# Kernel tuning notes

Hardware: AMD Instinct MI355X
Metric: run time of the kernel (lower is better)

The kernel has to match this reference:

```python
import jax, jax.numpy as jnp
import numpy as np

FACTOR = 5

def setup_inputs() -> dict:
    key = jax.random.key(0)
    k1, k2, k3, k4 = jax.random.split(key, 4)
    B, L, H, D = 4, 2048, 8, 64
    sample_k = min(FACTOR * int(np.ceil(np.log(L))), L)  # 40
    return {
        "queries": jax.random.normal(k1, (B, L, H, D), dtype=jnp.float32),
        "keys": jax.random.normal(k2, (B, L, H, D), dtype=jnp.float32),
        "values": jax.random.normal(k3, (B, L, H, D), dtype=jnp.float32),
        "index_sample": jax.random.randint(k4, (L, sample_k), 0, L, dtype=jnp.int32),
    }

def reference(queries, keys, values, index_sample):
    # [B, L, H, D] -> [B, H, L, D]
    Q = jnp.transpose(queries, (0, 2, 1, 3))
    K = jnp.transpose(keys, (0, 2, 1, 3))
    V = jnp.transpose(values, (0, 2, 1, 3))
    B, H, L_Q, D = Q.shape
    L_K = K.shape[2]
    u = min(FACTOR * int(np.ceil(np.log(L_Q))), L_Q)  # n_top

    # --- _prob_QK: sampled QK scores ---
    # K_sample: [B, H, L_Q, sample_k, D]
    K_sample = K[:, :, index_sample, :]
    # Q_K_sample[b,h,l,s] = Q[b,h,l,:] . K_sample[b,h,l,s,:]
    Q_K_sample = jnp.einsum('bhld,bhlsd->bhls', Q, K_sample)
    # sparsity measure M: max - mean over L_K
    M = Q_K_sample.max(axis=-1) - Q_K_sample.sum(axis=-1) / L_K  # [B,H,L_Q]
    _, M_top = jax.lax.top_k(M, u)  # [B,H,u]

    # reduced Q -> full scores against all keys
    Q_reduce = jnp.take_along_axis(Q, M_top[..., None], axis=2)  # [B,H,u,D]
    scores = jnp.einsum('bhud,bhkd->bhuk', Q_reduce, K)  # [B,H,u,L_K]
    scale = 1.0 / jnp.sqrt(jnp.asarray(D, dtype=scores.dtype))
    scores = scores * scale

    # --- initial context: mean of V over keys (mask_flag=False) ---
    V_mean = V.mean(axis=-2)  # [B,H,D]
    context = jnp.broadcast_to(V_mean[:, :, None, :], (B, H, L_Q, D))

    # --- update context at top-u query positions ---
    attn = jax.nn.softmax(scores, axis=-1)  # [B,H,u,L_K]
    ctx_top = jnp.einsum('bhuk,bhkd->bhud', attn, V)  # [B,H,u,D]
    b_idx = jnp.arange(B)[:, None, None]
    h_idx = jnp.arange(H)[None, :, None]
    context = context.at[b_idx, h_idx, M_top].set(ctx_top)
    return context  # [B, H, L_Q, D]
```

## Files before the change

kernel.cpp:

```cpp
#include <hip/hip_runtime.h>
#include <math.h>

#define LL 2048
#define HH 8
#define DD 64
#define SK 40
#define UU 40
#define SCALE 0.125f

__device__ __forceinline__ float dot4(float4 a, float4 b) {
  return a.x * b.x + a.y * b.y + a.z * b.z + a.w * b.w;
}


__global__ __launch_bounds__(512, 4) void k_A(
    const float* __restrict__ Q, const float* __restrict__ K,
    const float* __restrict__ V, const int* __restrict__ idxs,
    float* __restrict__ Mout, float* __restrict__ part)
{
  int bx = blockIdx.x;
  int t = threadIdx.x;

  if (bx < 2048) {
    __shared__ int sidx[4 * SK];
    __shared__ float wred[2][4][2][8];

    int xcd = bx & 7, slot = bx >> 3;
    int b = xcd >> 1;
    int l0 = ((xcd & 1) << 10) | (slot << 2);
    int w = t >> 6, lane = t & 63;
    int lpos = w >> 1, half = w & 1;
    int l = l0 + lpos;
    int h = (lane >> 2) & 7, dg = lane & 3, sp = lane >> 5;

    if (t < 4 * SK) sidx[t] = idxs[l0 * SK + t];

    const float4* Q4 = (const float4*)Q;
    int qb = (((b << 11) + l) << 7) + (h << 4) + dg;
    float4 q0 = Q4[qb], q1 = Q4[qb + 4], q2 = Q4[qb + 8], q3 = Q4[qb + 12];

    const float4* K4 = (const float4*)K;
    int kbb = (b << 18) + (h << 4) + dg;

    __syncthreads();

    const int* hidx = &sidx[lpos * SK + half * 20];
    float mx = -INFINITY, sum = 0.f;
#pragma unroll
    for (int pp = 0; pp < 10; pp += 2) {
      int i0 = hidx[pp * 2 + sp];
      int i1 = hidx[pp * 2 + 2 + sp];
      int o0 = kbb + (i0 << 7);
      int o1 = kbb + (i1 << 7);
      float4 a0 = K4[o0], a1 = K4[o0 + 4], a2 = K4[o0 + 8], a3 = K4[o0 + 12];
      float4 c0 = K4[o1], c1 = K4[o1 + 4], c2 = K4[o1 + 8], c3 = K4[o1 + 12];
      float p = dot4(q0, a0) + dot4(q1, a1) + dot4(q2, a2) + dot4(q3, a3);
      float r = dot4(q0, c0) + dot4(q1, c1) + dot4(q2, c2) + dot4(q3, c3);
      p += __shfl_xor(p, 1); p += __shfl_xor(p, 2);
      r += __shfl_xor(r, 1); r += __shfl_xor(r, 2);
      mx = fmaxf(mx, fmaxf(p, r));
      sum += p + r;
    }
    mx = fmaxf(mx, __shfl_xor(mx, 32));
    sum += __shfl_xor(sum, 32);
    if ((lane & 35) == 0) {
      wred[0][lpos][half][h] = mx;
      wred[1][lpos][half][h] = sum;
    }
    __syncthreads();
    if (t < 32) {
      int lp = t >> 3, hh = t & 7;
      float M0 = fmaxf(wred[0][lp][0][hh], wred[0][lp][1][hh]);
      float S0 = wred[1][lp][0][hh] + wred[1][lp][1][hh];
      Mout[((b * HH + hh) << 11) + (l0 + lp)] = M0 - S0 * (1.0f / (float)LL);
    }
  } else {
    __shared__ float sm[8][64];
    int blk = bx - 2048;
    int bh = blk >> 3, c = blk & 7;
    int b = bh >> 3, h = bh & 7;
    int w = t >> 6, d = t & 63;
    int l0 = (c << 8) + (w << 5);
    int base = (b << 20) + (l0 << 9) + (h << 6) + d;
    float a0 = 0, a1 = 0, a2 = 0, a3 = 0;
#pragma unroll
    for (int j = 0; j < 32; j += 4) {
      a0 += V[base + ((j + 0) << 9)];
      a1 += V[base + ((j + 1) << 9)];
      a2 += V[base + ((j + 2) << 9)];
      a3 += V[base + ((j + 3) << 9)];
    }
    sm[w][d] = a0 + a1 + a2 + a3;
    __syncthreads();
    if (t < 64) {
      float s = 0;
#pragma unroll
      for (int i = 0; i < 8; ++i) s += sm[i][t];
      part[(blk << 6) + t] = s;
    }
  }
}

__global__ __launch_bounds__(256) void k_B(
    const float* __restrict__ Mv, int* __restrict__ Mtop,
    const float4* __restrict__ part4, float4* __restrict__ out4)
{
  int bx = blockIdx.x;
  int t = threadIdx.x;

  if (bx < 32) {
    __shared__ float sv[LL];
    __shared__ float wm[4];
    __shared__ int wi[4];
    int bh = bx;
    int w = t >> 6, ln = t & 63;
    for (int i = t; i < LL; i += 256) sv[i] = Mv[bh * LL + i];
    __syncthreads();
    for (int r = 0; r < UU; ++r) {
      float bv = -INFINITY; int bi = 0;
#pragma unroll
      for (int j = 0; j < 8; ++j) {
        int i = t + (j << 8);
        float v = sv[i];
        if (v > bv) { bv = v; bi = i; }
      }
#pragma unroll
      for (int off = 1; off < 64; off <<= 1) {
        float ov = __shfl_xor(bv, off);
        int oi = __shfl_xor(bi, off);
        if (ov > bv || (ov == bv && oi < bi)) { bv = ov; bi = oi; }
      }
      if (ln == 0) { wm[w] = bv; wi[w] = bi; }
      __syncthreads();
      if (t == 0) {
        float Bv = wm[0]; int Bi = wi[0];
#pragma unroll
        for (int k = 1; k < 4; ++k)
          if (wm[k] > Bv || (wm[k] == Bv && wi[k] < Bi)) { Bv = wm[k]; Bi = wi[k]; }
        Mtop[bh * UU + r] = Bi;
        sv[Bi] = -INFINITY;
      }
      __syncthreads();
    }
  } else {
    __shared__ float4 vm[16];
    int i = (bx - 32) * 256 + t;
    int bh = i >> 15;
    if (t < 16) {
      int d4 = t;
      float4 s = {0, 0, 0, 0};
#pragma unroll
      for (int c = 0; c < 8; ++c) {
        float4 p = part4[((bh << 3) + c) * 16 + d4];
        s.x += p.x; s.y += p.y; s.z += p.z; s.w += p.w;
      }
      const float inv = 1.0f / (float)LL;
      s.x *= inv; s.y *= inv; s.z *= inv; s.w *= inv;
      vm[d4] = s;
    }
    __syncthreads();
    out4[i] = vm[i & 15];
  }
}

__global__ __launch_bounds__(512) void k_attn2(
    const float* __restrict__ Q, const float* __restrict__ K,
    const float* __restrict__ V, const int* __restrict__ Mtop,
    float* __restrict__ pm, float* __restrict__ pl, float4* __restrict__ pO4)
{
  __shared__ float4 Ks4[1024];
  __shared__ float Ps[8][256];
  __shared__ float4 Os4[4][2][4][16];
  __shared__ int gqi[8];

  int bx = blockIdx.x;
  int ch = bx & 7;
  int slot = bx >> 3;
  int bh = slot / 5, rg = slot % 5;
  int b = bh >> 3, h = bh & 7;
  int t = threadIdx.x;
  int w = t >> 6, ln = t & 63;
  int l0 = ch << 8;

  if (t < 8) gqi[t] = Mtop[bh * UU + rg * 8 + t];
  __syncthreads();

  float4 qv[16];
  {
    const float4* qrow = (const float4*)Q + (((b << 11) + gqi[w]) << 7) + (h << 4);
#pragma unroll
    for (int i = 0; i < 16; ++i) qv[i] = qrow[i];
  }

  const float4* K4 = (const float4*)K;
  int kbase = (((b << 11) + l0) << 7) + (h << 4);
  int col0 = t >> 4, d40 = t & 15;
  int sw0 = col0 * 16 + (d40 ^ (col0 & 7));
  float4 g0 = K4[kbase + col0 * 128 + d40];
  float4 g1 = K4[kbase + (col0 + 32) * 128 + d40];

  float sc[4];
#pragma unroll
  for (int st = 0; st < 4; ++st) {
    __syncthreads();
    Ks4[sw0] = g0;
    Ks4[sw0 + 512] = g1;
    float4 n0, n1;
    if (st < 3) {
      int lr = (st + 1) * 64;
      n0 = K4[kbase + (lr + col0) * 128 + d40];
      n1 = K4[kbase + (lr + col0 + 32) * 128 + d40];
    }
    __syncthreads();
    float s = 0.f;
#pragma unroll
    for (int d4 = 0; d4 < 16; ++d4) {
      float4 kv = Ks4[ln * 16 + (d4 ^ (ln & 7))];
      s += qv[d4].x * kv.x + qv[d4].y * kv.y + qv[d4].z * kv.z + qv[d4].w * kv.w;
    }
    sc[st] = s * SCALE;
    g0 = n0; g1 = n1;
  }

  float m = fmaxf(fmaxf(sc[0], sc[1]), fmaxf(sc[2], sc[3]));
#pragma unroll
  for (int off = 1; off < 64; off <<= 1) m = fmaxf(m, __shfl_xor(m, off));
  float lsum = 0.f;
#pragma unroll
  for (int st = 0; st < 4; ++st) {
    float p = __expf(sc[st] - m);
    Ps[w][st * 64 + ln] = p;
    lsum += p;
  }
#pragma unroll
  for (int off = 1; off < 64; off <<= 1) lsum += __shfl_xor(lsum, off);
  if (ln == 0) {
    int prow = bh * UU + rg * 8 + w;
    pm[prow * 8 + ch] = m;
    pl[prow * 8 + ch] = lsum;
  }
  __syncthreads();

  int rw = w >> 2, cq = w & 3;
  int cg = ln >> 4, d4 = ln & 15;
  float4 o0 = {0,0,0,0}, o1 = {0,0,0,0}, o2 = {0,0,0,0}, o3 = {0,0,0,0};
  int vb = (((b << 11) + l0 + cq * 64) << 7) + (h << 4);
  const float4* V4 = (const float4*)V;
#pragma unroll
  for (int i = 0; i < 16; ++i) {
    int c = i * 4 + cg;
    float4 v4 = V4[vb + c * 128 + d4];
    float p0 = Ps[rw * 4 + 0][cq * 64 + c];
    float p1 = Ps[rw * 4 + 1][cq * 64 + c];
    float p2 = Ps[rw * 4 + 2][cq * 64 + c];
    float p3 = Ps[rw * 4 + 3][cq * 64 + c];
    o0.x += p0 * v4.x; o0.y += p0 * v4.y; o0.z += p0 * v4.z; o0.w += p0 * v4.w;
    o1.x += p1 * v4.x; o1.y += p1 * v4.y; o1.z += p1 * v4.z; o1.w += p1 * v4.w;
    o2.x += p2 * v4.x; o2.y += p2 * v4.y; o2.z += p2 * v4.z; o2.w += p2 * v4.w;
    o3.x += p3 * v4.x; o3.y += p3 * v4.y; o3.z += p3 * v4.z; o3.w += p3 * v4.w;
  }
#pragma unroll
  for (int off = 16; off <= 32; off <<= 1) {
    o0.x += __shfl_xor(o0.x, off); o0.y += __shfl_xor(o0.y, off);
    o0.z += __shfl_xor(o0.z, off); o0.w += __shfl_xor(o0.w, off);
    o1.x += __shfl_xor(o1.x, off); o1.y += __shfl_xor(o1.y, off);
    o1.z += __shfl_xor(o1.z, off); o1.w += __shfl_xor(o1.w, off);
    o2.x += __shfl_xor(o2.x, off); o2.y += __shfl_xor(o2.y, off);
    o2.z += __shfl_xor(o2.z, off); o2.w += __shfl_xor(o2.w, off);
    o3.x += __shfl_xor(o3.x, off); o3.y += __shfl_xor(o3.y, off);
    o3.z += __shfl_xor(o3.z, off); o3.w += __shfl_xor(o3.w, off);
  }
  if (cg == 0) {
    Os4[cq][rw][0][d4] = o0;
    Os4[cq][rw][1][d4] = o1;
    Os4[cq][rw][2][d4] = o2;
    Os4[cq][rw][3][d4] = o3;
  }
  __syncthreads();

  if (t < 128) {
    int r = t >> 4, dd = t & 15;
    float4 a = Os4[0][r >> 2][r & 3][dd];
    float4 bq = Os4[1][r >> 2][r & 3][dd];
    float4 cc = Os4[2][r >> 2][r & 3][dd];
    float4 dq = Os4[3][r >> 2][r & 3][dd];
    float4 s;
    s.x = a.x + bq.x + cc.x + dq.x;
    s.y = a.y + bq.y + cc.y + dq.y;
    s.z = a.z + bq.z + cc.z + dq.z;
    s.w = a.w + bq.w + cc.w + dq.w;
    int prow = bh * UU + rg * 8 + r;
    pO4[(prow * 8 + ch) * 16 + dd] = s;
  }
}

__global__ __launch_bounds__(256) void k_comb(
    const float* __restrict__ pm, const float* __restrict__ pl,
    const float* __restrict__ pO, const int* __restrict__ Mtop,
    float* __restrict__ out)
{
  int row = blockIdx.x * 4 + (threadIdx.x >> 6);
  int ln = threadIdx.x & 63;
  int bh = row / UU, r40 = row % UU;
  float mm[8];
#pragma unroll
  for (int c = 0; c < 8; ++c) mm[c] = pm[row * 8 + c];
  float ms = mm[0];
#pragma unroll
  for (int c = 1; c < 8; ++c) ms = fmaxf(ms, mm[c]);
  float wsum = 0.f, o = 0.f;
#pragma unroll
  for (int c = 0; c < 8; ++c) {
    float wc = __expf(mm[c] - ms);
    wsum += wc * pl[row * 8 + c];
    o += wc * pO[(row * 8 + c) * 64 + ln];
  }
  int gq = Mtop[bh * UU + r40];
  out[((bh * LL + gq) << 6) + ln] = o / wsum;
}

extern "C" void kernel_launch(void* const* d_in, const int* in_sizes, int n_in,
                              void* d_out, int out_size, void* d_ws, size_t ws_size,
                              hipStream_t stream)
{
  (void)in_sizes; (void)n_in; (void)out_size; (void)ws_size;
  const float* Q = (const float*)d_in[0];
  const float* K = (const float*)d_in[1];
  const float* V = (const float*)d_in[2];
  const int* idxs = (const int*)d_in[3];
  float* out = (float*)d_out;

  float* wsf = (float*)d_ws;
  float* M     = wsf;
  float* part  = wsf + 65536;
  int*   Mtop  = (int*)(wsf + 83968);
  float* pm    = wsf + 85248;
  float* pl    = wsf + 95488;
  float* pO    = wsf + 105728;

  k_A    <<<2304, 512, 0, stream>>>(Q, K, V, idxs, M, part);
  k_B    <<<4128, 256, 0, stream>>>(M, Mtop, (const float4*)part, (float4*)out);
  k_attn2<<<1280, 512, 0, stream>>>(Q, K, V, Mtop, pm, pl, (float4*)pO);
  k_comb <<<320,  256, 0, stream>>>(pm, pl, pO, Mtop, out);
}
```

Before: 202.7 us.

## Fuse four kernels into one cooperative persistent kernel with grid syncs

Merges the four kernel launches into one cooperative kernel of 256 persistent blocks that loop over the old work items and separate the phases with grid-wide syncs. Shared memory is a union across phases. The goal is to remove launch overhead and the inter-kernel gaps, with a non-cooperative four-kernel fallback if the cooperative launch fails. The cost is lower parallelism per phase, since only 256 blocks loop over 2304 or 1280 work items. Grid syncs and per-iteration __syncthreads also add overhead, and the top-k phase runs on only 32 blocks while the others handle the fill.

```diff
diff --git a/kernel.cpp b/kernel.cpp
--- a/kernel.cpp
+++ b/kernel.cpp
@@ -1,5 +1,8 @@
 #include <hip/hip_runtime.h>
+#include <hip/hip_cooperative_groups.h>
 #include <math.h>
+
+namespace cg = cooperative_groups;
 
 #define LL 2048
 #define HH 8
@@ -13,181 +16,178 @@
 }
 
 
-__global__ __launch_bounds__(512, 4) void k_A(
-    const float* __restrict__ Q, const float* __restrict__ K,
-    const float* __restrict__ V, const int* __restrict__ idxs,
-    float* __restrict__ Mout, float* __restrict__ part)
-{
-  int bx = blockIdx.x;
-  int t = threadIdx.x;
-
-  if (bx < 2048) {
-    __shared__ int sidx[4 * SK];
-    __shared__ float wred[2][4][2][8];
-
-    int xcd = bx & 7, slot = bx >> 3;
-    int b = xcd >> 1;
-    int l0 = ((xcd & 1) << 10) | (slot << 2);
-    int w = t >> 6, lane = t & 63;
-    int lpos = w >> 1, half = w & 1;
-    int l = l0 + lpos;
-    int h = (lane >> 2) & 7, dg = lane & 3, sp = lane >> 5;
-
-    if (t < 4 * SK) sidx[t] = idxs[l0 * SK + t];
-
-    const float4* Q4 = (const float4*)Q;
-    int qb = (((b << 11) + l) << 7) + (h << 4) + dg;
-    float4 q0 = Q4[qb], q1 = Q4[qb + 4], q2 = Q4[qb + 8], q3 = Q4[qb + 12];
-
-    const float4* K4 = (const float4*)K;
-    int kbb = (b << 18) + (h << 4) + dg;
-
+struct SmemM   { int sidx[4 * SK]; float wred[2][4][2][8]; };
+struct SmemVP  { float sm[8][64]; };
+struct SmemTK  { float sv[LL]; float wm[8]; int wi[8]; };
+struct SmemFill{ float4 vm[16]; };
+struct SmemAttn{ float4 Ks4[1024]; float Ps[8][256]; float4 Os4[4][2][4][16]; int gqi[8]; };
+union SmemAll {
+  SmemM m; SmemVP vp; SmemTK tk; SmemFill fl; SmemAttn at;
+};
+
+__device__ void phase_m(SmemAll& S, int v, int t,
+                        const float* __restrict__ Q, const float* __restrict__ K,
+                        const int* __restrict__ idxs, float* __restrict__ Mout)
+{
+  __syncthreads();
+  int xcd = v & 7, slot = v >> 3;
+  int b = xcd >> 1;
+  int l0 = ((xcd & 1) << 10) | (slot << 2);
+  int w = t >> 6, lane = t & 63;
+  int lpos = w >> 1, half = w & 1;
+  int l = l0 + lpos;
+  int h = (lane >> 2) & 7, dg = lane & 3, sp = lane >> 5;
+
+  if (t < 4 * SK) S.m.sidx[t] = idxs[l0 * SK + t];
+
+  const float4* Q4 = (const float4*)Q;
+  int qb = (((b << 11) + l) << 7) + (h << 4) + dg;
+  float4 q0 = Q4[qb], q1 = Q4[qb + 4], q2 = Q4[qb + 8], q3 = Q4[qb + 12];
+
+  const float4* K4 = (const float4*)K;
+  int kbb = (b << 18) + (h << 4) + dg;
+
+  __syncthreads();
+
+  const int* hidx = &S.m.sidx[lpos * SK + half * 20];
+  float mx = -INFINITY, sum = 0.f;
+#pragma unroll
+  for (int pp = 0; pp < 10; pp += 2) {
+    int i0 = hidx[pp * 2 + sp];
+    int i1 = hidx[pp * 2 + 2 + sp];
+    int o0 = kbb + (i0 << 7);
+    int o1 = kbb + (i1 << 7);
+    float4 a0 = K4[o0], a1 = K4[o0 + 4], a2 = K4[o0 + 8], a3 = K4[o0 + 12];
+    float4 c0 = K4[o1], c1 = K4[o1 + 4], c2 = K4[o1 + 8], c3 = K4[o1 + 12];
+    float p = dot4(q0, a0) + dot4(q1, a1) + dot4(q2, a2) + dot4(q3, a3);
+    float r2 = dot4(q0, c0) + dot4(q1, c1) + dot4(q2, c2) + dot4(q3, c3);
+    p += __shfl_xor(p, 1); p += __shfl_xor(p, 2);
+    r2 += __shfl_xor(r2, 1); r2 += __shfl_xor(r2, 2);
+    mx = fmaxf(mx, fmaxf(p, r2));
+    sum += p + r2;
+  }
+  mx = fmaxf(mx, __shfl_xor(mx, 32));
+  sum += __shfl_xor(sum, 32);
+  if ((lane & 35) == 0) {
+    S.m.wred[0][lpos][half][h] = mx;
+    S.m.wred[1][lpos][half][h] = sum;
+  }
+  __syncthreads();
+  if (t < 32) {
+    int lp = t >> 3, hh = t & 7;
+    float M0 = fmaxf(S.m.wred[0][lp][0][hh], S.m.wred[0][lp][1][hh]);
+    float S0 = S.m.wred[1][lp][0][hh] + S.m.wred[1][lp][1][hh];
+    Mout[((b * HH + hh) << 11) + (l0 + lp)] = M0 - S0 * (1.0f / (float)LL);
+  }
+}
+
+__device__ void phase_vpart(SmemAll& S, int blk, int t,
+                            const float* __restrict__ V, float* __restrict__ part)
+{
+  __syncthreads();
+  int bh = blk >> 3, c = blk & 7;
+  int b = bh >> 3, h = bh & 7;
+  int w = t >> 6, d = t & 63;
+  int l0 = (c << 8) + (w << 5);
+  int base = (b << 20) + (l0 << 9) + (h << 6) + d;
+  float a0 = 0, a1 = 0, a2 = 0, a3 = 0;
+#pragma unroll
+  for (int j = 0; j < 32; j += 4) {
+    a0 += V[base + ((j + 0) << 9)];
+    a1 += V[base + ((j + 1) << 9)];
+    a2 += V[base + ((j + 2) << 9)];
+    a3 += V[base + ((j + 3) << 9)];
+  }
+  S.vp.sm[w][d] = a0 + a1 + a2 + a3;
+  __syncthreads();
+  if (t < 64) {
+    float s = 0;
+#pragma unroll
+    for (int i = 0; i < 8; ++i) s += S.vp.sm[i][t];
+    part[(blk << 6) + t] = s;
+  }
+}
+
+__device__ void phase_topk(SmemAll& S, int bh, int t,
+                           const float* __restrict__ Mv, int* __restrict__ Mtop)
+{
+  __syncthreads();
+  int w = t >> 6, ln = t & 63;
+  for (int i = t; i < LL; i += 512) S.tk.sv[i] = Mv[bh * LL + i];
+  __syncthreads();
+  for (int r = 0; r < UU; ++r) {
+    float bv = -INFINITY; int bi = 0;
+#pragma unroll
+    for (int j = 0; j < 4; ++j) {
+      int i = t + (j << 9);
+      float vv = S.tk.sv[i];
+      if (vv > bv) { bv = vv; bi = i; }
+    }
+#pragma unroll
+    for (int off = 1; off < 64; off <<= 1) {
+      float ov = __shfl_xor(bv, off);
+      int oi = __shfl_xor(bi, off);
+      if (ov > bv || (ov == bv && oi < bi)) { bv = ov; bi = oi; }
+    }
+    if (ln == 0) { S.tk.wm[w] = bv; S.tk.wi[w] = bi; }
     __syncthreads();
-
-    const int* hidx = &sidx[lpos * SK + half * 20];
-    float mx = -INFINITY, sum = 0.f;
-#pragma unroll
-    for (int pp = 0; pp < 10; pp += 2) {
-      int i0 = hidx[pp * 2 + sp];
-      int i1 = hidx[pp * 2 + 2 + sp];
-      int o0 = kbb + (i0 << 7);
-      int o1 = kbb + (i1 << 7);
-      float4 a0 = K4[o0], a1 = K4[o0 + 4], a2 = K4[o0 + 8], a3 = K4[o0 + 12];
-      float4 c0 = K4[o1], c1 = K4[o1 + 4], c2 = K4[o1 + 8], c3 = K4[o1 + 12];
-      float p = dot4(q0, a0) + dot4(q1, a1) + dot4(q2, a2) + dot4(q3, a3);
-      float r = dot4(q0, c0) + dot4(q1, c1) + dot4(q2, c2) + dot4(q3, c3);
-      p += __shfl_xor(p, 1); p += __shfl_xor(p, 2);
-      r += __shfl_xor(r, 1); r += __shfl_xor(r, 2);
-      mx = fmaxf(mx, fmaxf(p, r));
-      sum += p + r;
-    }
-    mx = fmaxf(mx, __shfl_xor(mx, 32));
-    sum += __shfl_xor(sum, 32);
-    if ((lane & 35) == 0) {
-      wred[0][lpos][half][h] = mx;
-      wred[1][lpos][half][h] = sum;
+    if (t == 0) {
+      float Bv = S.tk.wm[0]; int Bi = S.tk.wi[0];
+#pragma unroll
+      for (int k2 = 1; k2 < 8; ++k2)
+        if (S.tk.wm[k2] > Bv || (S.tk.wm[k2] == Bv && S.tk.wi[k2] < Bi)) { Bv = S.tk.wm[k2]; Bi = S.tk.wi[k2]; }
+      Mtop[bh * UU + r] = Bi;
+      S.tk.sv[Bi] = -INFINITY;
     }
     __syncthreads();
-    if (t < 32) {
-      int lp = t >> 3, hh = t & 7;
-      float M0 = fmaxf(wred[0][lp][0][hh], wred[0][lp][1][hh]);
-      float S0 = wred[1][lp][0][hh] + wred[1][lp][1][hh];
-      Mout[((b * HH + hh) << 11) + (l0 + lp)] = M0 - S0 * (1.0f / (float)LL);
-    }
-  } else {
-    __shared__ float sm[8][64];
-    int blk = bx - 2048;
-    int bh = blk >> 3, c = blk & 7;
-    int b = bh >> 3, h = bh & 7;
-    int w = t >> 6, d = t & 63;
-    int l0 = (c << 8) + (w << 5);
-    int base = (b << 20) + (l0 << 9) + (h << 6) + d;
-    float a0 = 0, a1 = 0, a2 = 0, a3 = 0;
-#pragma unroll
-    for (int j = 0; j < 32; j += 4) {
-      a0 += V[base + ((j + 0) << 9)];
-      a1 += V[base + ((j + 1) << 9)];
-      a2 += V[base + ((j + 2) << 9)];
-      a3 += V[base + ((j + 3) << 9)];
-    }
-    sm[w][d] = a0 + a1 + a2 + a3;
-    __syncthreads();
-    if (t < 64) {
-      float s = 0;
-#pragma unroll
-      for (int i = 0; i < 8; ++i) s += sm[i][t];
-      part[(blk << 6) + t] = s;
-    }
-  }
-}
-
-__global__ __launch_bounds__(256) void k_B(
-    const float* __restrict__ Mv, int* __restrict__ Mtop,
-    const float4* __restrict__ part4, float4* __restrict__ out4)
-{
-  int bx = blockIdx.x;
-  int t = threadIdx.x;
-
-  if (bx < 32) {
-    __shared__ float sv[LL];
-    __shared__ float wm[4];
-    __shared__ int wi[4];
-    int bh = bx;
-    int w = t >> 6, ln = t & 63;
-    for (int i = t; i < LL; i += 256) sv[i] = Mv[bh * LL + i];
-    __syncthreads();
-    for (int r = 0; r < UU; ++r) {
-      float bv = -INFINITY; int bi = 0;
-#pragma unroll
-      for (int j = 0; j < 8; ++j) {
-        int i = t + (j << 8);
-        float v = sv[i];
-        if (v > bv) { bv = v; bi = i; }
-      }
-#pragma unroll
-      for (int off = 1; off < 64; off <<= 1) {
-        float ov = __shfl_xor(bv, off);
-        int oi = __shfl_xor(bi, off);
-        if (ov > bv || (ov == bv && oi < bi)) { bv = ov; bi = oi; }
-      }
-      if (ln == 0) { wm[w] = bv; wi[w] = bi; }
-      __syncthreads();
-      if (t == 0) {
-        float Bv = wm[0]; int Bi = wi[0];
-#pragma unroll
-        for (int k = 1; k < 4; ++k)
-          if (wm[k] > Bv || (wm[k] == Bv && wi[k] < Bi)) { Bv = wm[k]; Bi = wi[k]; }
-        Mtop[bh * UU + r] = Bi;
-        sv[Bi] = -INFINITY;
-      }
-      __syncthreads();
-    }
-  } else {
-    __shared__ float4 vm[16];
-    int i = (bx - 32) * 256 + t;
-    int bh = i >> 15;
-    if (t < 16) {
-      int d4 = t;
-      float4 s = {0, 0, 0, 0};
-#pragma unroll
-      for (int c = 0; c < 8; ++c) {
-        float4 p = part4[((bh << 3) + c) * 16 + d4];
-        s.x += p.x; s.y += p.y; s.z += p.z; s.w += p.w;
-      }
-      const float inv = 1.0f / (float)LL;
-      s.x *= inv; s.y *= inv; s.z *= inv; s.w *= inv;
-      vm[d4] = s;
-    }
-    __syncthreads();
-    out4[i] = vm[i & 15];
-  }
-}
-
-__global__ __launch_bounds__(512) void k_attn2(
-    const float* __restrict__ Q, const float* __restrict__ K,
-    const float* __restrict__ V, const int* __restrict__ Mtop,
-    float* __restrict__ pm, float* __restrict__ pl, float4* __restrict__ pO4)
-{
-  __shared__ float4 Ks4[1024];
-  __shared__ float Ps[8][256];
-  __shared__ float4 Os4[4][2][4][16];
-  __shared__ int gqi[8];
-
-  int bx = blockIdx.x;
-  int ch = bx & 7;
-  int slot = bx >> 3;
+  }
+}
+
+__device__ void phase_fill(SmemAll& S, int v, int t,
+                           const float4* __restrict__ part4, float4* __restrict__ out4)
+{
+  __syncthreads();
+  int bh = v >> 4;
+  if (t < 16) {
+    float4 s = {0, 0, 0, 0};
+#pragma unroll
+    for (int c = 0; c < 8; ++c) {
+      float4 p = part4[((bh << 3) + c) * 16 + t];
+      s.x += p.x; s.y += p.y; s.z += p.z; s.w += p.w;
+    }
+    const float inv = 1.0f / (float)LL;
+    s.x *= inv; s.y *= inv; s.z *= inv; s.w *= inv;
+    S.fl.vm[t] = s;
+  }
+  __syncthreads();
+  int base = v << 11;
+#pragma unroll
+  for (int j = 0; j < 4; ++j) {
+    int i = base + (j << 9) + t;
+    out4[i] = S.fl.vm[i & 15];
+  }
+}
+
+__device__ void phase_attn(SmemAll& S, int v, int t,
+                           const float* __restrict__ Q, const float* __restrict__ K,
+                           const float* __restrict__ V, const int* __restrict__ Mtop,
+                           float* __restrict__ pm, float* __restrict__ pl,
+                           float4* __restrict__ pO4)
+{
+  __syncthreads();
+  int ch = v & 7;
+  int slot = v >> 3;
   int bh = slot / 5, rg = slot % 5;
   int b = bh >> 3, h = bh & 7;
-  int t = threadIdx.x;
   int w = t >> 6, ln = t & 63;
   int l0 = ch << 8;
 
-  if (t < 8) gqi[t] = Mtop[bh * UU + rg * 8 + t];
+  if (t < 8) S.at.gqi[t] = Mtop[bh * UU + rg * 8 + t];
   __syncthreads();
 
   float4 qv[16];
   {
-    const float4* qrow = (const float4*)Q + (((b << 11) + gqi[w]) << 7) + (h << 4);
+    const float4* qrow = (const float4*)Q + (((b << 11) + S.at.gqi[w]) << 7) + (h << 4);
 #pragma unroll
     for (int i = 0; i < 16; ++i) qv[i] = qrow[i];
   }
@@ -203,8 +203,8 @@
 #pragma unroll
   for (int st = 0; st < 4; ++st) {
     __syncthreads();
-    Ks4[sw0] = g0;
-    Ks4[sw0 + 512] = g1;
+    S.at.Ks4[sw0] = g0;
+    S.at.Ks4[sw0 + 512] = g1;
     float4 n0, n1;
     if (st < 3) {
       int lr = (st + 1) * 64;
@@ -215,7 +215,7 @@
     float s = 0.f;
 #pragma unroll
     for (int d4 = 0; d4 < 16; ++d4) {
-      float4 kv = Ks4[ln * 16 + (d4 ^ (ln & 7))];
+      float4 kv = S.at.Ks4[ln * 16 + (d4 ^ (ln & 7))];
       s += qv[d4].x * kv.x + qv[d4].y * kv.y + qv[d4].z * kv.z + qv[d4].w * kv.w;
     }
     sc[st] = s * SCALE;
@@ -229,7 +229,7 @@
 #pragma unroll
   for (int st = 0; st < 4; ++st) {
     float p = __expf(sc[st] - m);
-    Ps[w][st * 64 + ln] = p;
+    S.at.Ps[w][st * 64 + ln] = p;
     lsum += p;
   }
 #pragma unroll
@@ -242,18 +242,18 @@
   __syncthreads();
 
   int rw = w >> 2, cq = w & 3;
-  int cg = ln >> 4, d4 = ln & 15;
+  int cg2 = ln >> 4, d4 = ln & 15;
   float4 o0 = {0,0,0,0}, o1 = {0,0,0,0}, o2 = {0,0,0,0}, o3 = {0,0,0,0};
   int vb = (((b << 11) + l0 + cq * 64) << 7) + (h << 4);
   const float4* V4 = (const float4*)V;
 #pragma unroll
   for (int i = 0; i < 16; ++i) {
-    int c = i * 4 + cg;
+    int c = i * 4 + cg2;
     float4 v4 = V4[vb + c * 128 + d4];
-    float p0 = Ps[rw * 4 + 0][cq * 64 + c];
-    float p1 = Ps[rw * 4 + 1][cq * 64 + c];
-    float p2 = Ps[rw * 4 + 2][cq * 64 + c];
-    float p3 = Ps[rw * 4 + 3][cq * 64 + c];
+    float p0 = S.at.Ps[rw * 4 + 0][cq * 64 + c];
+    float p1 = S.at.Ps[rw * 4 + 1][cq * 64 + c];
+    float p2 = S.at.Ps[rw * 4 + 2][cq * 64 + c];
+    float p3 = S.at.Ps[rw * 4 + 3][cq * 64 + c];
     o0.x += p0 * v4.x; o0.y += p0 * v4.y; o0.z += p0 * v4.z; o0.w += p0 * v4.w;
     o1.x += p1 * v4.x; o1.y += p1 * v4.y; o1.z += p1 * v4.z; o1.w += p1 * v4.w;
     o2.x += p2 * v4.x; o2.y += p2 * v4.y; o2.z += p2 * v4.z; o2.w += p2 * v4.w;
@@ -270,20 +270,20 @@
     o3.x += __shfl_xor(o3.x, off); o3.y += __shfl_xor(o3.y, off);
     o3.z += __shfl_xor(o3.z, off); o3.w += __shfl_xor(o3.w, off);
   }
-  if (cg == 0) {
-    Os4[cq][rw][0][d4] = o0;
-    Os4[cq][rw][1][d4] = o1;
-    Os4[cq][rw][2][d4] = o2;
-    Os4[cq][rw][3][d4] = o3;
+  if (cg2 == 0) {
+    S.at.Os4[cq][rw][0][d4] = o0;
+    S.at.Os4[cq][rw][1][d4] = o1;
+    S.at.Os4[cq][rw][2][d4] = o2;
+    S.at.Os4[cq][rw][3][d4] = o3;
   }
   __syncthreads();
 
   if (t < 128) {
     int r = t >> 4, dd = t & 15;
-    float4 a = Os4[0][r >> 2][r & 3][dd];
-    float4 bq = Os4[1][r >> 2][r & 3][dd];
-    float4 cc = Os4[2][r >> 2][r & 3][dd];
-    float4 dq = Os4[3][r >> 2][r & 3][dd];
+    float4 a  = S.at.Os4[0][r >> 2][r & 3][dd];
+    float4 bq = S.at.Os4[1][r >> 2][r & 3][dd];
+    float4 cc = S.at.Os4[2][r >> 2][r & 3][dd];
+    float4 dq = S.at.Os4[3][r >> 2][r & 3][dd];
     float4 s;
     s.x = a.x + bq.x + cc.x + dq.x;
     s.y = a.y + bq.y + cc.y + dq.y;
@@ -294,13 +294,13 @@
   }
 }
 
-__global__ __launch_bounds__(256) void k_comb(
-    const float* __restrict__ pm, const float* __restrict__ pl,
-    const float* __restrict__ pO, const int* __restrict__ Mtop,
-    float* __restrict__ out)
-{
-  int row = blockIdx.x * 4 + (threadIdx.x >> 6);
-  int ln = threadIdx.x & 63;
+__device__ void phase_comb(int v, int t,
+                           const float* __restrict__ pm, const float* __restrict__ pl,
+                           const float* __restrict__ pO, const int* __restrict__ Mtop,
+                           float* __restrict__ out)
+{
+  int row = v * 8 + (t >> 6);
+  int ln = t & 63;
   int bh = row / UU, r40 = row % UU;
   float mm[8];
 #pragma unroll
@@ -317,6 +317,75 @@
   }
   int gq = Mtop[bh * UU + r40];
   out[((bh * LL + gq) << 6) + ln] = o / wsum;
+}
+
+__global__ __launch_bounds__(512, 2) void k_mega(
+    const float* __restrict__ Q, const float* __restrict__ K,
+    const float* __restrict__ V, const int* __restrict__ idxs,
+    float* __restrict__ M, float* __restrict__ part, int* __restrict__ Mtop,
+    float* __restrict__ pm, float* __restrict__ pl, float* __restrict__ pO,
+    float* __restrict__ out)
+{
+  __shared__ SmemAll S;
+  cg::grid_group gg = cg::this_grid();
+  int r = blockIdx.x, t = threadIdx.x;
+  const int G = 256;
+
+  for (int v = r; v < 2304; v += G) {
+    if (v < 2048) phase_m(S, v, t, Q, K, idxs, M);
+    else          phase_vpart(S, v - 2048, t, V, part);
+  }
+  gg.sync();
+
+  if (r < 32) {
+    phase_topk(S, r, t, M, Mtop);
+  } else {
+    for (int v = r - 32; v < 512; v += G - 32)
+      phase_fill(S, v, t, (const float4*)part, (float4*)out);
+  }
+  gg.sync();
+
+  for (int v = r; v < 1280; v += G)
+    phase_attn(S, v, t, Q, K, V, Mtop, pm, pl, (float4*)pO);
+  gg.sync();
+
+  for (int v = r; v < 160; v += G)
+    phase_comb(v, t, pm, pl, pO, Mtop, out);
+}
+
+__global__ __launch_bounds__(512, 2) void k_f1(
+    const float* __restrict__ Q, const float* __restrict__ K,
+    const float* __restrict__ V, const int* __restrict__ idxs,
+    float* __restrict__ M, float* __restrict__ part)
+{
+  __shared__ SmemAll S;
+  int v = blockIdx.x, t = threadIdx.x;
+  if (v < 2048) phase_m(S, v, t, Q, K, idxs, M);
+  else          phase_vpart(S, v - 2048, t, V, part);
+}
+__global__ __launch_bounds__(512, 2) void k_f2(
+    const float* __restrict__ M, int* __restrict__ Mtop,
+    const float4* __restrict__ part4, float4* __restrict__ out4)
+{
+  __shared__ SmemAll S;
+  int v = blockIdx.x, t = threadIdx.x;
+  if (v < 32) phase_topk(S, v, t, M, Mtop);
+  else        phase_fill(S, v - 32, t, part4, out4);
+}
+__global__ __launch_bounds__(512, 2) void k_f3(
+    const float* __restrict__ Q, const float* __restrict__ K,
+    const float* __restrict__ V, const int* __restrict__ Mtop,
+    float* __restrict__ pm, float* __restrict__ pl, float4* __restrict__ pO4)
+{
+  __shared__ SmemAll S;
+  phase_attn(S, blockIdx.x, threadIdx.x, Q, K, V, Mtop, pm, pl, pO4);
+}
+__global__ __launch_bounds__(512, 2) void k_f4(
+    const float* __restrict__ pm, const float* __restrict__ pl,
+    const float* __restrict__ pO, const int* __restrict__ Mtop,
+    float* __restrict__ out)
+{
+  phase_comb(blockIdx.x, threadIdx.x, pm, pl, pO, Mtop, out);
 }
 
 extern "C" void kernel_launch(void* const* d_in, const int* in_sizes, int n_in,
@@ -338,8 +407,16 @@
   float* pl    = wsf + 95488;
   float* pO    = wsf + 105728;
 
-  k_A    <<<2304, 512, 0, stream>>>(Q, K, V, idxs, M, part);
-  k_B    <<<4128, 256, 0, stream>>>(M, Mtop, (const float4*)part, (float4*)out);
-  k_attn2<<<1280, 512, 0, stream>>>(Q, K, V, Mtop, pm, pl, (float4*)pO);
-  k_comb <<<320,  256, 0, stream>>>(pm, pl, pO, Mtop, out);
-}
+  void* args[] = { (void*)&Q, (void*)&K, (void*)&V, (void*)&idxs,
+                   (void*)&M, (void*)&part, (void*)&Mtop,
+                   (void*)&pm, (void*)&pl, (void*)&pO, (void*)&out };
+  hipError_t e = hipLaunchCooperativeKernel((const void*)k_mega, dim3(256), dim3(512),
+                                            args, 0, stream);
+  if (e != hipSuccess) {
+    (void)hipGetLastError();
+    k_f1<<<2304, 512, 0, stream>>>(Q, K, V, idxs, M, part);
+    k_f2<<<544,  512, 0, stream>>>(M, Mtop, (const float4*)part, (float4*)out);
+    k_f3<<<1280, 512, 0, stream>>>(Q, K, V, Mtop, pm, pl, (float4*)pO);
+    k_f4<<<160,  512, 0, stream>>>(pm, pl, pO, Mtop, out);
+  }
+}
```

Measured after the change: 336.6 us. +66.0%, slower.
